# Kernel optimization log

Measured on AMD Instinct MI355X. Metric: run time of the kernel, lower is better.

Reference implementation:

```python
import jax, jax.numpy as jnp
import numpy as np

BS = 32  # block size
EPS = 1e-5

def _bn(h, g, b):
    # training-mode batchnorm over (N,H,W) of the gathered block batch
    mu = h.mean((0, 2, 3), keepdims=True)
    var = h.var((0, 2, 3), keepdims=True)
    return (h - mu) * jax.lax.rsqrt(var + EPS) * g.reshape(1, -1, 1, 1) + b.reshape(1, -1, 1, 1)

def setup_inputs() -> dict:
    key = jax.random.key(0)
    ks = jax.random.split(key, 12)
    B, Cin, H, W, Cout = 4, 128, 256, 256, 256
    Hb, Wb = H // BS, W // BS
    x = jax.random.normal(ks[0], (B, Cin, H, W), dtype=jnp.float32)
    rng = np.random.default_rng(0)
    flat = np.sort(rng.choice(B * Hb * Wb, size=128, replace=False)).astype(np.int32)
    bi = flat // (Hb * Wb)
    by = (flat % (Hb * Wb)) // Wb
    bx = flat % Wb
    block_idx = jnp.asarray(np.stack([bi, by, bx], axis=1), dtype=jnp.int32)  # [Nact,3]
    s1 = 1.0 / np.sqrt(Cin)
    s2 = 1.0 / np.sqrt(Cout * 9)
    return {
        "x": x,
        "w1": jax.random.normal(ks[1], (Cout, Cin), jnp.float32) * s1,
        "b1": jnp.zeros((Cout,), jnp.float32),
        "g1": jnp.ones((Cout,), jnp.float32),
        "be1": jnp.zeros((Cout,), jnp.float32),
        "w2": jax.random.normal(ks[2], (Cout, Cout, 3, 3), jnp.float32) * s2,
        "b2": jnp.zeros((Cout,), jnp.float32),
        "g2": jnp.ones((Cout,), jnp.float32),
        "be2": jnp.zeros((Cout,), jnp.float32),
        "wd": jax.random.normal(ks[3], (Cout, Cin), jnp.float32) * s1,
        "bd": jnp.zeros((Cout,), jnp.float32),
        "block_idx": block_idx,
    }

def reference(x, w1, b1, g1, be1, w2, b2, g2, be2, wd, bd, block_idx):
    B, Cin, H, W = x.shape
    Cout = w1.shape[0]
    Hb, Wb = H // BS, W // BS
    # --- sparse gather: [Nact, Cin, BS, BS] ---
    xb = x.reshape(B, Cin, Hb, BS, Wb, BS).transpose(0, 2, 4, 1, 3, 5)
    xb = xb.reshape(B * Hb * Wb, Cin, BS, BS)
    flat = block_idx[:, 0] * (Hb * Wb) + block_idx[:, 1] * Wb + block_idx[:, 2]
    dense = xb[flat]
    # --- dense conv stack on active blocks ---
    h = jnp.einsum('nchw,oc->nohw', dense, w1) + b1.reshape(1, -1, 1, 1)
    h = jax.nn.relu(_bn(h, g1, be1))  # relu is inplace in torch -> feeds conv2
    h = jax.lax.conv_general_dilated(h, w2, (1, 1), 'SAME',
                                     dimension_numbers=('NCHW', 'OIHW', 'NCHW'))
    h = h + b2.reshape(1, -1, 1, 1)
    dense_y = jax.nn.relu(_bn(h, g2, be2))
    # NOTE: original conv3/bn3 output is dead code (scatter uses dense_y); omitted.
    # --- dense base path (in_channels != out_channels -> downsample 1x1 conv) ---
    ybase = jnp.einsum('nchw,oc->nohw', x, wd) + bd.reshape(1, -1, 1, 1)
    # --- sparse scatter (overwrite, add=False) ---
    yb = ybase.reshape(B, Cout, Hb, BS, Wb, BS).transpose(0, 2, 4, 1, 3, 5)
    yb = yb.reshape(B * Hb * Wb, Cout, BS, BS)
    yb = yb.at[flat].set(dense_y)
    y = yb.reshape(B, Hb, Wb, Cout, BS, BS).transpose(0, 3, 1, 4, 2, 5)
    return y.reshape(B, Cout, H, W)
```

## Files before the change

### kernel.cpp

```cpp
#include <hip/hip_runtime.h>
#include <stdint.h>

#define CIN  128
#define COUT 256
#define HH   256
#define WW   256
#define BSZ  32
#define HB   8
#define WB   8
#define NBLK 256
#define P2   34
#define PIX2 1156

typedef __attribute__((ext_vector_type(8))) short bfx8;
typedef __attribute__((ext_vector_type(4))) float f32x4;

#define MFMA(a,b,c) __builtin_amdgcn_mfma_f32_16x16x32_bf16((a),(b),(c),0,0,0)

typedef const __attribute__((address_space(1))) unsigned int gu32;
typedef __attribute__((address_space(3))) unsigned int lu32;
#define GLOAD16(g, p) __builtin_amdgcn_global_load_lds((gu32*)(g), (lu32*)(p), 16, 0, 0)

static __device__ __forceinline__ float bf2f(unsigned short u){
  union { unsigned int i; float f; } v; v.i = ((unsigned int)u)<<16; return v.f;
}
static __device__ __forceinline__ unsigned short f2bf(float f){
  union { float f; unsigned int i; } v; v.f = f;
  unsigned int r = v.i + 0x7fffu + ((v.i>>16)&1u);
  return (unsigned short)(r>>16);
}

__global__ void k_prep(const float* __restrict__ w1, const float* __restrict__ wd,
                       const float* __restrict__ w2,
                       unsigned short* __restrict__ w1b, unsigned short* __restrict__ wdb,
                       unsigned short* __restrict__ w2t){
  int i = blockIdx.x*256 + threadIdx.x;
  if (i < COUT*CIN){ w1b[i] = f2bf(w1[i]); wdb[i] = f2bf(wd[i]); }
  if (i < COUT*COUT*9){
    int co = i/2304, r = i - co*2304;
    int ci = r/9,   tp = r - ci*9;
    w2t[((size_t)tp*COUT + co)*COUT + ci] = f2bf(w2[i]);
  }
}

__global__ void k_lists(const int* __restrict__ bidx, int nact,
                        int* __restrict__ flags, int* __restrict__ inact){
  int t = threadIdx.x;
  if (t < nact){
    int f = bidx[t*3]*(HB*WB) + bidx[t*3+1]*WB + bidx[t*3+2];
    flags[f] = 1;
  }
  __syncthreads();
  if (t == 0){
    int c = 0;
    for (int f = 0; f < NBLK; ++f) if (!flags[f]) inact[c++] = f;
  }
}

template<int MODE>
__global__ __launch_bounds__(256) void k_gemm1(
    const float* __restrict__ x, const unsigned short* __restrict__ wgt,
    const int* __restrict__ bidx, const int* __restrict__ inact,
    const float* __restrict__ bd, unsigned short* __restrict__ h1p,
    float* __restrict__ out, float* __restrict__ part){
  __shared__ unsigned short lds[2*5120];
  int rg = blockIdx.x, cot = blockIdx.y, z = blockIdx.z;
  int bi, by, bx;
  if (MODE == 0){ bi = bidx[z*3]; by = bidx[z*3+1]; bx = bidx[z*3+2]; }
  else { int fl = inact[z]; bi = fl>>6; by = (fl>>3)&7; bx = fl&7; }
  int t = threadIdx.x, l = t&63, wid = t>>6;
  int wc = wid>>1, wp = wid&1;
  int y0 = rg*4;
  int co_w = cot*128 + wc*64;

  const unsigned short* wb = wgt + (size_t)(co_w + (l&15))*CIN + ((l>>4)*8);
  bfx8 wfrag[4][4];
  #pragma unroll
  for (int kc = 0; kc < 4; ++kc)
    #pragma unroll
    for (int m = 0; m < 4; ++m)
      wfrag[kc][m] = *(const bfx8*)(wb + kc*32 + (size_t)m*16*CIN);

  const float* xb = x + (size_t)bi*CIN*HH*WW + (size_t)(by*BSZ + y0)*WW + bx*BSZ;
  float4 ra[2], rb_[2];
  auto ldreg = [&](int kc){
    #pragma unroll
    for (int j = 0; j < 2; ++j){
      int u = j*256 + t;
      int ci0 = (u>>5)*2 + kc*32;
      int p = (u&31)*4;
      const float* s = xb + (size_t)ci0*(HH*WW) + (p>>5)*WW + (p&31);
      ra[j]  = *(const float4*)s;
      rb_[j] = *(const float4*)(s + HH*WW);
    }
  };
  auto wrlds = [&](int buf){
    #pragma unroll
    for (int j = 0; j < 2; ++j){
      int u = j*256 + t;
      int ci0 = (u>>5)*2;
      int p = (u&31)*4;
      unsigned short* d = &lds[buf*5120 + ci0];
      *(ushort2*)&d[(p+0)*40] = make_ushort2(f2bf(ra[j].x), f2bf(rb_[j].x));
      *(ushort2*)&d[(p+1)*40] = make_ushort2(f2bf(ra[j].y), f2bf(rb_[j].y));
      *(ushort2*)&d[(p+2)*40] = make_ushort2(f2bf(ra[j].z), f2bf(rb_[j].z));
      *(ushort2*)&d[(p+3)*40] = make_ushort2(f2bf(ra[j].w), f2bf(rb_[j].w));
    }
  };

  f32x4 acc[4][4] = {};
  ldreg(0);
  for (int kc = 0; kc < 4; ++kc){
    wrlds(kc&1);
    if (kc < 3) ldreg(kc+1);
    __syncthreads();
    const unsigned short* lb = &lds[(kc&1)*5120];
    #pragma unroll
    for (int f = 0; f < 4; ++f){
      bfx8 b = *(const bfx8*)&lb[(wp*64 + f*16 + (l&15))*40 + (l>>4)*8];
      acc[0][f] = MFMA(wfrag[kc][0], b, acc[0][f]);
      acc[1][f] = MFMA(wfrag[kc][1], b, acc[1][f]);
      acc[2][f] = MFMA(wfrag[kc][2], b, acc[2][f]);
      acc[3][f] = MFMA(wfrag[kc][3], b, acc[3][f]);
    }
  }

  #pragma unroll
  for (int m = 0; m < 4; ++m){
    int co = co_w + m*16 + ((l>>4)<<2);
    #pragma unroll
    for (int f = 0; f < 4; ++f){
      int px = wp*64 + f*16 + (l&15);
      int ly = px>>5, lx = px&31;
      if (MODE == 0){
        *(ushort4*)&h1p[((size_t)z*PIX2 + (size_t)(y0+ly+1)*P2 + (lx+1))*COUT + co] =
          make_ushort4(f2bf(acc[m][f][0]), f2bf(acc[m][f][1]),
                       f2bf(acc[m][f][2]), f2bf(acc[m][f][3]));
      } else {
        int gy = by*BSZ + y0 + ly, gx = bx*BSZ + lx;
        #pragma unroll
        for (int j = 0; j < 4; ++j)
          out[(((size_t)bi*COUT + co + j)*HH + gy)*WW + gx] = acc[m][f][j] + bd[co+j];
      }
    }
  }

  if (MODE == 0){
    int hwi = rg*2 + cot;
    #pragma unroll
    for (int pass = 0; pass < 2; ++pass){
      int j = pass*8 + (t>>5);
      if (j < 9){
        int hp = hwi*9 + j;
        if (hp < 132){
          int r, c;
          if (hp < 34){ r = 0; c = hp; }
          else if (hp < 68){ r = 33; c = hp - 34; }
          else if (hp < 100){ r = hp - 67; c = 0; }
          else { r = hp - 99; c = 33; }
          bfx8 z8 = {};
          *(bfx8*)&h1p[((size_t)z*PIX2 + (size_t)r*P2 + c)*COUT + (t&31)*8] = z8;
        }
      }
    }

    float s_[4][4], q_[4][4];
    #pragma unroll
    for (int m = 0; m < 4; ++m)
      #pragma unroll
      for (int j = 0; j < 4; ++j){
        float s = 0.f, q = 0.f;
        #pragma unroll
        for (int f = 0; f < 4; ++f){ float v = acc[m][f][j]; s += v; q += v*v; }
        s_[m][j] = s; q_[m][j] = q;
      }
    #pragma unroll
    for (int off = 1; off < 16; off <<= 1)
      #pragma unroll
      for (int m = 0; m < 4; ++m)
        #pragma unroll
        for (int j = 0; j < 4; ++j){
          s_[m][j] += __shfl_xor(s_[m][j], off);
          q_[m][j] += __shfl_xor(q_[m][j], off);
        }
    if ((l&15) == 0){
      int grp = z & 15;
      #pragma unroll
      for (int m = 0; m < 4; ++m)
        #pragma unroll
        for (int j = 0; j < 4; ++j){
          int co = co_w + m*16 + ((l>>4)<<2) + j;
          atomicAdd(&part[((size_t)grp*COUT + co)*2],   s_[m][j]);
          atomicAdd(&part[((size_t)grp*COUT + co)*2+1], q_[m][j]);
        }
    }
  }
}

__global__ void k_fin(const float* __restrict__ part, const float* __restrict__ g,
                      const float* __restrict__ be, float* __restrict__ st, float inv){
  int t = threadIdx.x;
  float s = 0.f, q = 0.f;
  #pragma unroll
  for (int gi = 0; gi < 16; ++gi){
    s += part[((size_t)gi*COUT + t)*2];
    q += part[((size_t)gi*COUT + t)*2+1];
  }
  float mu = s*inv, var = q*inv - mu*mu;
  float sc = g[t]*rsqrtf(var + 1e-5f);
  st[t] = sc; st[256+t] = be[t] - mu*sc;
}

__global__ void k_bn1(unsigned short* __restrict__ h1p, const float* __restrict__ st){
  int t = threadIdx.x;
  int ci0 = (t&31)*8;
  float sc[8], tc[8];
  #pragma unroll
  for (int j = 0; j < 8; ++j){ sc[j] = st[ci0+j]; tc[j] = st[256+ci0+j]; }
  #pragma unroll
  for (int it = 0; it < 4; ++it){
    int gp = blockIdx.x*32 + it*8 + (t>>5);
    int n = gp >> 10, p = gp & 1023;
    int row = (p>>5) + 1, col = (p&31) + 1;
    unsigned short* addr = h1p + ((size_t)n*PIX2 + (size_t)row*P2 + col)*COUT + ci0;
    bfx8 v = *(bfx8*)addr;
    unsigned short o[8];
    #pragma unroll
    for (int j = 0; j < 8; ++j){
      float f = bf2f(((unsigned short*)&v)[j]);
      o[j] = f2bf(fmaxf(f*sc[j] + tc[j], 0.f));
    }
    *(bfx8*)addr = *(bfx8*)o;
  }
}

__global__ __launch_bounds__(512, 4) void k_conv2(
    const unsigned short* __restrict__ h1p, const unsigned short* __restrict__ w2t,
    const int* __restrict__ bidx, float* __restrict__ out, float* __restrict__ part){
  __shared__ unsigned short lds[24576];
  int bxid = blockIdx.x, n = blockIdx.y;
  int h = bxid & 1, q = bxid >> 1;
  int bi = bidx[n*3], by = bidx[n*3+1], bx = bidx[n*3+2];
  int t = threadIdx.x, l = t&63, wid = t>>6;
  int wm = wid>>1, wn = wid&1;
  int y0 = q*8;

  int offA[4], offB[2];
  #pragma unroll
  for (int j = 0; j < 4; ++j){
    int i = j*512 + t;
    int row = i>>3, sl_ = i&7;
    offA[j] = row*COUT + (sl_ ^ (row&7))*8;
  }
  #pragma unroll
  for (int j = 0; j < 2; ++j){
    int i = j*512 + t;
    int row = i>>3, sl_ = i&7;
    offB[j] = ((row>>5)*P2 + (row&31))*COUT + (sl_ ^ (row&7))*8;
  }
  const unsigned short* h1q = h1p + ((size_t)n*PIX2 + (size_t)(y0 + h*4)*P2)*COUT;

  int lr = l&15, lh = l>>4;
  f32x4 acc[4][4] = {};

  for (int s = 0; s < 36; ++s){
    int tp = s>>2, cc = s&3;
    int dy = tp/3, dx = tp - dy*3;
    const unsigned short* wsrc = w2t + (size_t)tp*COUT*COUT + cc*64;
    const unsigned short* psrc = h1q + (size_t)(dy*P2 + dx)*COUT + cc*64;
    __syncthreads();
    #pragma unroll
    for (int j = 0; j < 4; ++j)
      GLOAD16(wsrc + offA[j], &lds[(j*512 + t)*8]);
    #pragma unroll
    for (int j = 0; j < 2; ++j)
      GLOAD16(psrc + offB[j], &lds[16384 + (j*512 + t)*8]);
    __syncthreads();
    #pragma unroll
    for (int kk = 0; kk < 2; ++kk){
      bfx8 af[4], bfr[4];
      #pragma unroll
      for (int m = 0; m < 4; ++m)
        af[m] = *(const bfx8*)&lds[(wm*64 + m*16 + lr)*64 + ((kk*4 + lh) ^ (lr&7))*8];
      #pragma unroll
      for (int nn = 0; nn < 4; ++nn)
        bfr[nn] = *(const bfx8*)&lds[16384 + (wn*64 + nn*16 + lr)*64 + ((kk*4 + lh) ^ (lr&7))*8];
      #pragma unroll
      for (int m = 0; m < 4; ++m)
        #pragma unroll
        for (int nn = 0; nn < 4; ++nn)
          acc[m][nn] = MFMA(af[m], bfr[nn], acc[m][nn]);
    }
  }

  #pragma unroll
  for (int m = 0; m < 4; ++m){
    int co = wm*64 + m*16 + lh*4;
    #pragma unroll
    for (int nn = 0; nn < 4; ++nn){
      int px = h*128 + wn*64 + nn*16 + lr;
      int gy = by*BSZ + y0 + (px>>5), gx = bx*BSZ + (px&31);
      #pragma unroll
      for (int j = 0; j < 4; ++j)
        out[(((size_t)bi*COUT + co + j)*HH + gy)*WW + gx] = acc[m][nn][j];
    }
  }

  #pragma unroll
  for (int m = 0; m < 4; ++m){
    #pragma unroll
    for (int j = 0; j < 4; ++j){
      float s = 0.f, qq = 0.f;
      #pragma unroll
      for (int nn = 0; nn < 4; ++nn){ float v = acc[m][nn][j]; s += v; qq += v*v; }
      #pragma unroll
      for (int off = 1; off < 16; off <<= 1){
        s  += __shfl_xor(s,  off);
        qq += __shfl_xor(qq, off);
      }
      if (lr == 0){
        int co = wm*64 + m*16 + lh*4 + j;
        atomicAdd(&part[((size_t)(n&15)*COUT + co)*2],   s);
        atomicAdd(&part[((size_t)(n&15)*COUT + co)*2+1], qq);
      }
    }
  }
}

__global__ void k_bn2(float* __restrict__ out, const int* __restrict__ bidx,
                      const float* __restrict__ st){
  int cq = blockIdx.x, n = blockIdx.y, t = threadIdx.x;
  int bi = bidx[n*3], by = bidx[n*3+1], bx = bidx[n*3+2];
  int px0 = t*4; int ly = px0>>5, lx = px0&31;
  float* base = out + (size_t)bi*COUT*HH*WW + (size_t)(by*BSZ+ly)*WW + bx*BSZ + lx;
  for (int c = 0; c < 64; ++c){
    int co = cq*64 + c;
    float sc = st[co], tc = st[256+co];
    float4* p = (float4*)(base + (size_t)co*HH*WW);
    float4 v = *p;
    v.x = fmaxf(v.x*sc+tc, 0.f); v.y = fmaxf(v.y*sc+tc, 0.f);
    v.z = fmaxf(v.z*sc+tc, 0.f); v.w = fmaxf(v.w*sc+tc, 0.f);
    *p = v;
  }
}

extern "C" void kernel_launch(void* const* d_in, const int* in_sizes, int n_in,
                              void* d_out, int out_size, void* d_ws, size_t ws_size,
                              hipStream_t stream){
  const float* x   = (const float*)d_in[0];
  const float* w1  = (const float*)d_in[1];
  const float* g1  = (const float*)d_in[3];
  const float* be1 = (const float*)d_in[4];
  const float* w2  = (const float*)d_in[5];
  const float* g2  = (const float*)d_in[7];
  const float* be2 = (const float*)d_in[8];
  const float* wd  = (const float*)d_in[9];
  const float* bd  = (const float*)d_in[10];
  const int* bidx  = (const int*)d_in[11];
  float* out = (float*)d_out;
  const int nact = in_sizes[11]/3;
  const int ninact = NBLK - nact;

  char* wsp = (char*)d_ws;
  size_t off = 0;
  auto carve = [&](size_t bytes)->char*{
    char* p = wsp + off; off += (bytes + 255) & ~(size_t)255; return p;
  };
  unsigned short* h1p = (unsigned short*)carve((size_t)nact*PIX2*COUT*2 + 4096);
  unsigned short* w1b = (unsigned short*)carve((size_t)COUT*CIN*2);
  unsigned short* wdb = (unsigned short*)carve((size_t)COUT*CIN*2);
  unsigned short* w2t = (unsigned short*)carve((size_t)9*COUT*COUT*2);
  float* s1t1  = (float*)carve(512*4);
  float* s2t2  = (float*)carve(512*4);
  float* part1 = (float*)carve((size_t)16*COUT*2*4);
  float* part2 = (float*)carve((size_t)16*COUT*2*4);
  int* flags   = (int*)carve(NBLK*4);
  int* inact   = (int*)carve(NBLK*4);

  hipMemsetAsync(flags, 0, NBLK*4, stream);
  hipMemsetAsync(part1, 0, (size_t)16*COUT*2*4, stream);
  hipMemsetAsync(part2, 0, (size_t)16*COUT*2*4, stream);
  k_lists<<<1, 256, 0, stream>>>(bidx, nact, flags, inact);
  k_prep<<<2304, 256, 0, stream>>>(w1, wd, w2, w1b, wdb, w2t);
  k_gemm1<0><<<dim3(8, 2, nact), 256, 0, stream>>>(x, w1b, bidx, inact, bd, h1p, out, part1);
  k_fin<<<1, 256, 0, stream>>>(part1, g1, be1, s1t1, 1.0f/((float)nact*1024.0f));
  k_bn1<<<dim3(nact*32), 256, 0, stream>>>(h1p, s1t1);
  k_conv2<<<dim3(8, nact), 512, 0, stream>>>(h1p, w2t, bidx, out, part2);
  k_fin<<<1, 256, 0, stream>>>(part2, g2, be2, s2t2, 1.0f/((float)nact*1024.0f));
  if (ninact > 0)
    k_gemm1<1><<<dim3(8, 2, ninact), 256, 0, stream>>>(x, wdb, bidx, inact, bd, h1p, out, part1);
  k_bn2<<<dim3(4, nact), 256, 0, stream>>>(out, bidx, s2t2);
}
```

Measured before the change: 428.0 us.

## Fold memsets and list build into prep kernel; load conv2 weights directly to registers

Merges the three memsets and the inactive-block list kernel into the weight-prep launch as extra blocks, removing four launches/ops from the stream. Separately, conv2 now reads the A (weight) fragments straight from global memory into registers instead of staging them through LDS, shrinking LDS from 48KB to 16KB to raise occupancy and cut LDS traffic. This trades coalesced async LDS loads for per-lane 16-byte global loads that rely on cache hits for weights shared across blocks.

```diff
diff --git a/kernel.cpp b/kernel.cpp
--- a/kernel.cpp
+++ b/kernel.cpp
@@ -33,27 +33,39 @@
 __global__ void k_prep(const float* __restrict__ w1, const float* __restrict__ wd,
                        const float* __restrict__ w2,
                        unsigned short* __restrict__ w1b, unsigned short* __restrict__ wdb,
-                       unsigned short* __restrict__ w2t){
-  int i = blockIdx.x*256 + threadIdx.x;
-  if (i < COUT*CIN){ w1b[i] = f2bf(w1[i]); wdb[i] = f2bf(wd[i]); }
-  if (i < COUT*COUT*9){
-    int co = i/2304, r = i - co*2304;
-    int ci = r/9,   tp = r - ci*9;
-    w2t[((size_t)tp*COUT + co)*COUT + ci] = f2bf(w2[i]);
-  }
-}
-
-__global__ void k_lists(const int* __restrict__ bidx, int nact,
-                        int* __restrict__ flags, int* __restrict__ inact){
-  int t = threadIdx.x;
-  if (t < nact){
-    int f = bidx[t*3]*(HB*WB) + bidx[t*3+1]*WB + bidx[t*3+2];
-    flags[f] = 1;
-  }
-  __syncthreads();
-  if (t == 0){
-    int c = 0;
-    for (int f = 0; f < NBLK; ++f) if (!flags[f]) inact[c++] = f;
+                       unsigned short* __restrict__ w2t,
+                       const int* __restrict__ bidx, int nact, int* __restrict__ inact,
+                       float* __restrict__ part1, float* __restrict__ part2){
+  __shared__ int fl[NBLK];
+  int bid = blockIdx.x, t = threadIdx.x;
+  if (bid < 2304){
+    int i = bid*256 + t;
+    if (i < COUT*CIN){ w1b[i] = f2bf(w1[i]); wdb[i] = f2bf(wd[i]); }
+    if (i < COUT*COUT*9){
+      int co = i/2304, r = i - co*2304;
+      int ci = r/9,   tp = r - ci*9;
+      w2t[((size_t)tp*COUT + co)*COUT + ci] = f2bf(w2[i]);
+    }
+  } else if (bid < 2308){
+    float4 z = make_float4(0.f,0.f,0.f,0.f);
+    float* p = part1 + ((size_t)(bid-2304)*256 + t)*8;
+    *(float4*)p = z; *(float4*)(p+4) = z;
+  } else if (bid < 2312){
+    float4 z = make_float4(0.f,0.f,0.f,0.f);
+    float* p = part2 + ((size_t)(bid-2308)*256 + t)*8;
+    *(float4*)p = z; *(float4*)(p+4) = z;
+  } else {
+    fl[t] = 0;
+    __syncthreads();
+    if (t < nact){
+      int f = bidx[t*3]*(HB*WB) + bidx[t*3+1]*WB + bidx[t*3+2];
+      fl[f] = 1;
+    }
+    __syncthreads();
+    if (t == 0){
+      int c = 0;
+      for (int f = 0; f < NBLK; ++f) if (!fl[f]) inact[c++] = f;
+    }
   }
 }
 
@@ -237,7 +249,7 @@
 __global__ __launch_bounds__(512, 4) void k_conv2(
     const unsigned short* __restrict__ h1p, const unsigned short* __restrict__ w2t,
     const int* __restrict__ bidx, float* __restrict__ out, float* __restrict__ part){
-  __shared__ unsigned short lds[24576];
+  __shared__ unsigned short lds[8192];
   int bxid = blockIdx.x, n = blockIdx.y;
   int h = bxid & 1, q = bxid >> 1;
   int bi = bidx[n*3], by = bidx[n*3+1], bx = bidx[n*3+2];
@@ -245,13 +257,7 @@
   int wm = wid>>1, wn = wid&1;
   int y0 = q*8;
 
-  int offA[4], offB[2];
-  #pragma unroll
-  for (int j = 0; j < 4; ++j){
-    int i = j*512 + t;
-    int row = i>>3, sl_ = i&7;
-    offA[j] = row*COUT + (sl_ ^ (row&7))*8;
-  }
+  int offB[2];
   #pragma unroll
   for (int j = 0; j < 2; ++j){
     int i = j*512 + t;
@@ -261,35 +267,39 @@
   const unsigned short* h1q = h1p + ((size_t)n*PIX2 + (size_t)(y0 + h*4)*P2)*COUT;
 
   int lr = l&15, lh = l>>4;
+  const unsigned short* aW = w2t + (size_t)(wm*64 + lr)*COUT + lh*8;
+
   f32x4 acc[4][4] = {};
 
   for (int s = 0; s < 36; ++s){
     int tp = s>>2, cc = s&3;
     int dy = tp/3, dx = tp - dy*3;
-    const unsigned short* wsrc = w2t + (size_t)tp*COUT*COUT + cc*64;
     const unsigned short* psrc = h1q + (size_t)(dy*P2 + dx)*COUT + cc*64;
-    __syncthreads();
-    #pragma unroll
-    for (int j = 0; j < 4; ++j)
-      GLOAD16(wsrc + offA[j], &lds[(j*512 + t)*8]);
+    const unsigned short* asrc = aW + (size_t)tp*COUT*COUT + cc*64;
+    __syncthreads();
     #pragma unroll
     for (int j = 0; j < 2; ++j)
-      GLOAD16(psrc + offB[j], &lds[16384 + (j*512 + t)*8]);
+      GLOAD16(psrc + offB[j], &lds[(j*512 + t)*8]);
+    bfx8 af[4][2];
+    #pragma unroll
+    for (int m = 0; m < 4; ++m)
+      #pragma unroll
+      for (int kk = 0; kk < 2; ++kk)
+        af[m][kk] = *(const bfx8*)(asrc + (size_t)(m*16)*COUT + kk*32);
     __syncthreads();
     #pragma unroll
     for (int kk = 0; kk < 2; ++kk){
-      bfx8 af[4], bfr[4];
+      bfx8 bfr[4];
+      #pragma unroll
+      for (int nn = 0; nn < 4; ++nn){
+        int r = wn*64 + nn*16 + lr;
+        bfr[nn] = *(const bfx8*)&lds[r*64 + (((kk*4 + lh) ^ (r&7))*8)];
+      }
       #pragma unroll
       for (int m = 0; m < 4; ++m)
-        af[m] = *(const bfx8*)&lds[(wm*64 + m*16 + lr)*64 + ((kk*4 + lh) ^ (lr&7))*8];
-      #pragma unroll
-      for (int nn = 0; nn < 4; ++nn)
-        bfr[nn] = *(const bfx8*)&lds[16384 + (wn*64 + nn*16 + lr)*64 + ((kk*4 + lh) ^ (lr&7))*8];
-      #pragma unroll
-      for (int m = 0; m < 4; ++m)
         #pragma unroll
         for (int nn = 0; nn < 4; ++nn)
-          acc[m][nn] = MFMA(af[m], bfr[nn], acc[m][nn]);
+          acc[m][nn] = MFMA(af[m][kk], bfr[nn], acc[m][nn]);
     }
   }
 
@@ -374,14 +384,10 @@
   float* s2t2  = (float*)carve(512*4);
   float* part1 = (float*)carve((size_t)16*COUT*2*4);
   float* part2 = (float*)carve((size_t)16*COUT*2*4);
-  int* flags   = (int*)carve(NBLK*4);
   int* inact   = (int*)carve(NBLK*4);
 
-  hipMemsetAsync(flags, 0, NBLK*4, stream);
-  hipMemsetAsync(part1, 0, (size_t)16*COUT*2*4, stream);
-  hipMemsetAsync(part2, 0, (size_t)16*COUT*2*4, stream);
-  k_lists<<<1, 256, 0, stream>>>(bidx, nact, flags, inact);
-  k_prep<<<2304, 256, 0, stream>>>(w1, wd, w2, w1b, wdb, w2t);
+  k_prep<<<2313, 256, 0, stream>>>(w1, wd, w2, w1b, wdb, w2t,
+                                   bidx, nact, inact, part1, part2);
   k_gemm1<0><<<dim3(8, 2, nact), 256, 0, stream>>>(x, w1b, bidx, inact, bd, h1p, out, part1);
   k_fin<<<1, 256, 0, stream>>>(part1, g1, be1, s1t1, 1.0f/((float)nact*1024.0f));
   k_bn1<<<dim3(nact*32), 256, 0, stream>>>(h1p, s1t1);
```

Result: slower. 578.5 us (+35.2%).
